# Kernel optimization log

Measured on AMD Instinct MI355X. Metric: run time of the kernel, lower is better.

Reference implementation:

```python
import jax, jax.numpy as jnp
import numpy as np

DIM = 768
HEADS = 12
HEAD_DIM = DIM // HEADS
SCALE = HEAD_DIM ** (-0.5)


def setup_inputs() -> dict:
    key = jax.random.key(0)
    k1, k2, k3, k4 = jax.random.split(key, 4)
    B, N = 2, 48 * 48
    x = jax.random.normal(k1, (B, N, DIM), dtype=jnp.float32)
    qkv_w = jax.random.normal(k2, (3 * DIM, DIM), dtype=jnp.float32) * (DIM ** -0.5)
    proj_w = jax.random.normal(k3, (DIM, DIM), dtype=jnp.float32) * (DIM ** -0.5)
    proj_b = jax.random.normal(k4, (DIM,), dtype=jnp.float32) * 0.02
    return {"x": x, "H": 48, "W": 48, "qkv_w": qkv_w, "proj_w": proj_w, "proj_b": proj_b}


def reference(x, H, W, qkv_w, proj_w, proj_b):
    B, N, C = x.shape
    h, d = HEADS, HEAD_DIM
    # qkv linear (no bias): [B,N,3C], then split into per-head q,k,v [B,h,N,d]
    qkv = jnp.einsum('bnc,fc->bnf', x, qkv_w)
    qkv = qkv.reshape(B, N, 3, h, d).transpose(2, 0, 3, 1, 4)
    q, k, v = qkv[0], qkv[1], qkv[2]
    attn = jnp.einsum('bhnd,bhmd->bhnm', q, k) * SCALE  # [B,h,N,N]
    attn = jax.nn.softmax(attn, axis=-1)
    out = jnp.einsum('bhnm,bhmd->bhnd', attn, v)  # [B,h,N,d]
    out = out.transpose(0, 2, 1, 3).reshape(B, N, C)
    out = jnp.einsum('bnc,fc->bnf', out, proj_w) + proj_b
    return out
```

## Files before the change

kernel.cpp:

```cpp
#include <hip/hip_runtime.h>

#define B_    2
#define N_    2304
#define C_    768
#define HEADS 12
#define D_    64
#define F3    2304
#define M_    (B_*N_)
#define SPLITS 2
#define KSPAN (N_/SPLITS)
#define QSCALE 0.18033688011112042f

typedef __attribute__((ext_vector_type(8)))  short bfrag;
typedef __attribute__((ext_vector_type(4)))  float ffrag;
typedef __attribute__((ext_vector_type(16))) float ffrag16;
typedef __attribute__((ext_vector_type(4)))  unsigned ufrag;

__device__ __forceinline__ short f2bf(float f) {
    unsigned u = __float_as_uint(f);
    u += 0x7fff + ((u >> 16) & 1);
    return (short)(u >> 16);
}

__device__ __forceinline__ void gl2lds16(const void* g, void* l) {
    __builtin_amdgcn_global_load_lds(
        (const __attribute__((address_space(1))) void*)g,
        (__attribute__((address_space(3))) void*)l, 16, 0, 0);
}

__device__ __forceinline__ unsigned pktrunc(float a, float b) {
    return __builtin_amdgcn_perm(__float_as_uint(a), __float_as_uint(b),
                                 0x03020706u);
}

__global__ __launch_bounds__(256) void cast_all(const float* __restrict__ x,
                                                const float* __restrict__ qw,
                                                const float* __restrict__ pw,
                                                short* __restrict__ dst) {
    const int nx4 = (M_*C_)/4, nq4 = (F3*C_)/4, np4 = (C_*C_)/4;
    int i = blockIdx.x * 256 + threadIdx.x;
    if (i >= nx4 + nq4 + np4) return;
    const float* src; int off;
    if (i < nx4)            { src = x;  off = i; }
    else if (i < nx4 + nq4) { src = qw; off = i - nx4; }
    else                    { src = pw; off = i - nx4 - nq4; }
    float4 v = ((const float4*)src)[off];
    short4 o;
    o.x = f2bf(v.x); o.y = f2bf(v.y); o.z = f2bf(v.z); o.w = f2bf(v.w);
    ((short4*)dst)[i] = o;
}

__global__ __launch_bounds__(256) void qkv_gemm(const short* __restrict__ xb,
                                                const short* __restrict__ wb,
                                                short* __restrict__ Qb,
                                                short* __restrict__ Kb,
                                                short* __restrict__ Vtb) {
    __shared__ short As[128*32];
    __shared__ short Bs[128*32];
    const int t = threadIdx.x;
    const int w = t >> 6, lane = t & 63;
    const int quad = lane >> 4, l15 = lane & 15;
    const int wr = w >> 1, wc = w & 1;
    const int m0 = blockIdx.y * 128, f0 = blockIdx.x * 128;

    ffrag acc[4][4] = {};

    for (int k0 = 0; k0 < C_; k0 += 32) {
        __syncthreads();
        #pragma unroll
        for (int r = 0; r < 2; ++r) {
            int seg = r*4 + w;
            int row = seg*16 + (lane >> 2);
            int kk  = (lane & 3) * 8;
            gl2lds16(xb + (size_t)(m0+row)*C_ + k0 + kk, As + seg*512);
            gl2lds16(wb + (size_t)(f0+row)*C_ + k0 + kk, Bs + seg*512);
        }
        __syncthreads();
        bfrag af[4], bf[4];
        #pragma unroll
        for (int i = 0; i < 4; ++i)
            af[i] = *(const bfrag*)(As + (wr*64 + i*16 + l15)*32 + quad*8);
        #pragma unroll
        for (int j = 0; j < 4; ++j)
            bf[j] = *(const bfrag*)(Bs + (wc*64 + j*16 + l15)*32 + quad*8);
        #pragma unroll
        for (int i = 0; i < 4; ++i)
            #pragma unroll
            for (int j = 0; j < 4; ++j)
                acc[i][j] = __builtin_amdgcn_mfma_f32_16x16x32_bf16(af[i], bf[j], acc[i][j], 0, 0, 0);
    }

    const int b   = m0 / N_;
    const int seg = f0 + wc*64;
    const int which = seg / C_;
    const int head  = (seg - which*C_) >> 6;
    const int bh    = b*HEADS + head;
    const int nbase = (m0 - b*N_) + wr*64 + quad*4;

    if (which == 0) {
        #pragma unroll
        for (int i = 0; i < 4; ++i) {
            int n0 = nbase + i*16;
            #pragma unroll
            for (int j = 0; j < 4; ++j) {
                int d = j*16 + l15;
                #pragma unroll
                for (int r = 0; r < 4; ++r)
                    Qb[((size_t)bh*N_ + n0 + r)*D_ + d] = f2bf(acc[i][j][r] * QSCALE);
            }
        }
    } else if (which == 1) {
        #pragma unroll
        for (int i = 0; i < 4; ++i) {
            int n0 = nbase + i*16;
            #pragma unroll
            for (int j = 0; j < 4; ++j) {
                int d = j*16 + l15;
                #pragma unroll
                for (int r = 0; r < 4; ++r)
                    Kb[((size_t)bh*N_ + n0 + r)*D_ + d] = f2bf(acc[i][j][r]);
            }
        }
    } else {
        #pragma unroll
        for (int i = 0; i < 4; ++i) {
            int n0 = nbase + i*16;
            #pragma unroll
            for (int j = 0; j < 4; ++j) {
                int d = j*16 + l15;
                short4 vv;
                vv.x = f2bf(acc[i][j][0]);
                vv.y = f2bf(acc[i][j][1]);
                vv.z = f2bf(acc[i][j][2]);
                vv.w = f2bf(acc[i][j][3]);
                *(short4*)(Vtb + ((size_t)bh*D_ + d)*N_ + n0) = vv;
            }
        }
    }
}

__global__ __launch_bounds__(128) void attn_mfma(const short* __restrict__ Qb,
                                                 const short* __restrict__ Kb,
                                                 const short* __restrict__ Vtb,
                                                 float* __restrict__ Opart,
                                                 float* __restrict__ lpart) {
    __shared__ short Qs[64*64];
    __shared__ short Ks[64*64];
    __shared__ short Vts[64*64];
    const int t = threadIdx.x;
    const int w = t >> 6, lane = t & 63;
    const int l31 = lane & 31, hi = lane >> 5;
    const int bh = blockIdx.x, q0 = blockIdx.y * 64;
    const int split = blockIdx.z;
    const int kbase = split * KSPAN;
    const size_t base = (size_t)bh * N_ * D_;
    const int lrow = lane >> 3;
    const int lc   = (lane & 7) ^ lrow;

    #pragma unroll
    for (int r = 0; r < 4; ++r) {
        int s = r*2 + w;
        int row = s*8 + lrow;
        gl2lds16(Qb + base + (size_t)(q0+row)*D_ + lc*8, Qs + s*512);
    }
    __syncthreads();

    bfrag qf[4];
    {
        int row = w*32 + l31, r7 = row & 7;
        #pragma unroll
        for (int kc = 0; kc < 4; ++kc)
            qf[kc] = *(const bfrag*)(Qs + row*64 + ((kc*2 + hi) ^ r7)*8);
    }

    bfrag vones;
    #pragma unroll
    for (int j = 0; j < 8; ++j) vones[j] = (short)0x3f80;

    ffrag16 oacc[2], lfr;
    #pragma unroll
    for (int r = 0; r < 16; ++r) { oacc[0][r] = 0.f; oacc[1][r] = 0.f; lfr[r] = 0.f; }

    for (int k0 = kbase; k0 < kbase + KSPAN; k0 += 64) {
        __syncthreads();
        #pragma unroll
        for (int r = 0; r < 4; ++r) {
            int s = r*2 + w;
            int row = s*8 + lrow;
            gl2lds16(Kb  + base + (size_t)(k0+row)*D_ + lc*8,    Ks  + s*512);
            gl2lds16(Vtb + (size_t)(bh*D_ + row)*N_ + k0 + lc*8, Vts + s*512);
        }
        __syncthreads();

        ufrag pfr[4];
        #pragma unroll
        for (int kt = 0; kt < 2; ++kt) {
            ffrag16 s;
            #pragma unroll
            for (int r = 0; r < 16; ++r) s[r] = 0.f;
            int row = kt*32 + l31, r7 = row & 7;
            #pragma unroll
            for (int kc = 0; kc < 4; ++kc) {
                bfrag kf = *(const bfrag*)(Ks + row*64 + ((kc*2 + hi) ^ r7)*8);
                s = __builtin_amdgcn_mfma_f32_32x32x16_bf16(kf, qf[kc], s, 0, 0, 0);
            }
            #pragma unroll
            for (int r = 0; r < 16; ++r)
                s[r] = __builtin_amdgcn_exp2f(s[r]);
            unsigned q01_0 = pktrunc(s[0],  s[1]),  q23_0 = pktrunc(s[2],  s[3]);
            unsigned q01_1 = pktrunc(s[4],  s[5]),  q23_1 = pktrunc(s[6],  s[7]);
            unsigned q01_2 = pktrunc(s[8],  s[9]),  q23_2 = pktrunc(s[10], s[11]);
            unsigned q01_3 = pktrunc(s[12], s[13]), q23_3 = pktrunc(s[14], s[15]);
            unsigned r0 = __shfl_xor(hi ? q01_0 : q01_1, 32, 64);
            unsigned r1 = __shfl_xor(hi ? q23_0 : q23_1, 32, 64);
            unsigned r2 = __shfl_xor(hi ? q01_2 : q01_3, 32, 64);
            unsigned r3 = __shfl_xor(hi ? q23_2 : q23_3, 32, 64);
            ufrag lo, hif;
            lo[0] = hi ? r0 : q01_0;  lo[1] = hi ? r1 : q23_0;
            lo[2] = hi ? q01_1 : r0;  lo[3] = hi ? q23_1 : r1;
            hif[0] = hi ? r2 : q01_2; hif[1] = hi ? r3 : q23_2;
            hif[2] = hi ? q01_3 : r2; hif[3] = hi ? q23_3 : r3;
            pfr[kt*2]     = lo;
            pfr[kt*2 + 1] = hif;
        }

        #pragma unroll
        for (int kc = 0; kc < 4; ++kc) {
            bfrag pf = __builtin_bit_cast(bfrag, pfr[kc]);
            #pragma unroll
            for (int dt = 0; dt < 2; ++dt) {
                int row = dt*32 + l31, r7 = row & 7;
                bfrag vf = *(const bfrag*)(Vts + row*64 + ((kc*2 + hi) ^ r7)*8);
                oacc[dt] = __builtin_amdgcn_mfma_f32_32x32x16_bf16(pf, vf, oacc[dt], 0, 0, 0);
            }
            lfr = __builtin_amdgcn_mfma_f32_32x32x16_bf16(pf, vones, lfr, 0, 0, 0);
        }
    }

    const int b = bh / HEADS, head = bh - b*HEADS;
    float* Op = Opart + (size_t)split * M_ * C_;
    float* lp = lpart + (size_t)split * (B_*HEADS) * N_;

    if (l31 == 0) {
        #pragma unroll
        for (int r = 0; r < 16; ++r) {
            int n = q0 + w*32 + (r & 3) + 8*(r >> 2) + 4*hi;
            lp[bh*N_ + n] = lfr[r];
        }
    }

    #pragma unroll
    for (int dt = 0; dt < 2; ++dt)
        #pragma unroll
        for (int r = 0; r < 16; ++r) {
            int n = q0 + w*32 + (r & 3) + 8*(r >> 2) + 4*hi;
            int c = head*D_ + dt*32 + l31;
            Op[((size_t)b*N_ + n)*C_ + c] = oacc[dt][r];
        }
}

__global__ __launch_bounds__(256) void attn_merge(const float* __restrict__ Opart,
                                                  const float* __restrict__ lpart,
                                                  short* __restrict__ Ob) {
    int i = blockIdx.x * 256 + threadIdx.x;
    int m = i / (C_/4);
    int c = (i - m*(C_/4)) * 4;
    int b = m / N_, n = m - b*N_;
    int bh = b*HEADS + (c >> 6);
    float4 o0 = ((const float4*)Opart)[i];
    float4 o1 = ((const float4*)(Opart + (size_t)M_*C_))[i];
    float l = lpart[bh*N_ + n] + lpart[(B_*HEADS)*N_ + bh*N_ + n];
    float inv = 1.f / l;
    short4 o;
    o.x = f2bf((o0.x + o1.x) * inv);
    o.y = f2bf((o0.y + o1.y) * inv);
    o.z = f2bf((o0.z + o1.z) * inv);
    o.w = f2bf((o0.w + o1.w) * inv);
    ((short4*)Ob)[i] = o;
}

__global__ __launch_bounds__(256) void proj_gemm(const short* __restrict__ Ab,
                                                 const short* __restrict__ wb,
                                                 const float* __restrict__ bias,
                                                 float* __restrict__ out) {
    __shared__ short As[128*32];
    __shared__ short Bs[128*32];
    const int t = threadIdx.x;
    const int w = t >> 6, lane = t & 63;
    const int quad = lane >> 4, l15 = lane & 15;
    const int wr = w >> 1, wc = w & 1;
    const int m0 = blockIdx.y * 128, f0 = blockIdx.x * 128;

    ffrag acc[4][4] = {};

    for (int k0 = 0; k0 < C_; k0 += 32) {
        __syncthreads();
        #pragma unroll
        for (int r = 0; r < 2; ++r) {
            int seg = r*4 + w;
            int row = seg*16 + (lane >> 2);
            int kk  = (lane & 3) * 8;
            gl2lds16(Ab + (size_t)(m0+row)*C_ + k0 + kk, As + seg*512);
            gl2lds16(wb + (size_t)(f0+row)*C_ + k0 + kk, Bs + seg*512);
        }
        __syncthreads();
        bfrag af[4], bf[4];
        #pragma unroll
        for (int i = 0; i < 4; ++i)
            af[i] = *(const bfrag*)(As + (wr*64 + i*16 + l15)*32 + quad*8);
        #pragma unroll
        for (int j = 0; j < 4; ++j)
            bf[j] = *(const bfrag*)(Bs + (wc*64 + j*16 + l15)*32 + quad*8);
        #pragma unroll
        for (int i = 0; i < 4; ++i)
            #pragma unroll
            for (int j = 0; j < 4; ++j)
                acc[i][j] = __builtin_amdgcn_mfma_f32_16x16x32_bf16(af[i], bf[j], acc[i][j], 0, 0, 0);
    }

    #pragma unroll
    for (int i = 0; i < 4; ++i) {
        int mbase = m0 + wr*64 + i*16 + quad*4;
        #pragma unroll
        for (int j = 0; j < 4; ++j) {
            int f = f0 + wc*64 + j*16 + l15;
            float bv = bias[f];
            #pragma unroll
            for (int r = 0; r < 4; ++r)
                out[(size_t)(mbase + r)*C_ + f] = acc[i][j][r] + bv;
        }
    }
}

extern "C" void kernel_launch(void* const* d_in, const int* in_sizes, int n_in,
                              void* d_out, int out_size, void* d_ws, size_t ws_size,
                              hipStream_t stream) {
    const float* x      = (const float*)d_in[0];
    const float* qkv_w  = (const float*)d_in[3];
    const float* proj_w = (const float*)d_in[4];
    const float* proj_b = (const float*)d_in[5];
    float* out = (float*)d_out;

    const size_t nx = (size_t)M_ * C_;
    const size_t nq = (size_t)F3 * C_;
    const size_t np = (size_t)C_ * C_;
    short* xb  = (short*)d_ws;
    short* qwb = xb  + nx;
    short* pwb = qwb + nq;
    short* Qb  = pwb + np;
    short* Kb  = Qb  + nx;
    short* Vtb = Kb  + nx;
    short* Ob  = Vtb + nx;
    float* Opart = (float*)(Ob + nx);
    float* lpart = Opart + (size_t)SPLITS * M_ * C_;

    const int ncast4 = (int)((nx + nq + np) / 4);
    cast_all<<<dim3((ncast4 + 255)/256), 256, 0, stream>>>(x, qkv_w, proj_w, xb);

    qkv_gemm<<<dim3(F3/128, M_/128), 256, 0, stream>>>(xb, qwb, Qb, Kb, Vtb);
    attn_mfma<<<dim3(B_*HEADS, N_/64, SPLITS), 128, 0, stream>>>(Qb, Kb, Vtb, Opart, lpart);
    attn_merge<<<dim3(((int)(nx/4) + 255)/256), 256, 0, stream>>>(Opart, lpart, Ob);
    proj_gemm<<<dim3(C_/128, M_/128), 256, 0, stream>>>(Ob, pwb, proj_b, out);
}
```

Measured before the change: 210.9 us.

## Widen K tiles in QKV GEMM and attention, add swizzled LDS layout

The QKV GEMM now stages a 64-wide K slice per iteration with an XOR-swizzled LDS layout, halving the number of barrier pairs and reducing bank conflicts. The attention kernel loads two 64-key K/V tiles per iteration into doubled LDS buffers, halving its sync count. It reuses the K buffer for the Q staging and adds a min-blocks-per-CU hint of 3. The cost is more LDS per block and possibly more register pressure under the occupancy hint.

```diff
diff --git a/kernel.cpp b/kernel.cpp
--- a/kernel.cpp
+++ b/kernel.cpp
@@ -55,39 +55,45 @@
                                                 short* __restrict__ Qb,
                                                 short* __restrict__ Kb,
                                                 short* __restrict__ Vtb) {
-    __shared__ short As[128*32];
-    __shared__ short Bs[128*32];
+    __shared__ short As[128*64];
+    __shared__ short Bs[128*64];
     const int t = threadIdx.x;
     const int w = t >> 6, lane = t & 63;
     const int quad = lane >> 4, l15 = lane & 15;
     const int wr = w >> 1, wc = w & 1;
     const int m0 = blockIdx.y * 128, f0 = blockIdx.x * 128;
+    const int lrow = lane >> 3;
+    const int lc   = (lane & 7) ^ lrow;
+    const int r7   = l15 & 7;
 
     ffrag acc[4][4] = {};
 
-    for (int k0 = 0; k0 < C_; k0 += 32) {
-        __syncthreads();
-        #pragma unroll
-        for (int r = 0; r < 2; ++r) {
+    for (int k0 = 0; k0 < C_; k0 += 64) {
+        __syncthreads();
+        #pragma unroll
+        for (int r = 0; r < 4; ++r) {
             int seg = r*4 + w;
-            int row = seg*16 + (lane >> 2);
-            int kk  = (lane & 3) * 8;
-            gl2lds16(xb + (size_t)(m0+row)*C_ + k0 + kk, As + seg*512);
-            gl2lds16(wb + (size_t)(f0+row)*C_ + k0 + kk, Bs + seg*512);
-        }
-        __syncthreads();
-        bfrag af[4], bf[4];
-        #pragma unroll
-        for (int i = 0; i < 4; ++i)
-            af[i] = *(const bfrag*)(As + (wr*64 + i*16 + l15)*32 + quad*8);
-        #pragma unroll
-        for (int j = 0; j < 4; ++j)
-            bf[j] = *(const bfrag*)(Bs + (wc*64 + j*16 + l15)*32 + quad*8);
-        #pragma unroll
-        for (int i = 0; i < 4; ++i)
+            int row = seg*8 + lrow;
+            gl2lds16(xb + (size_t)(m0+row)*C_ + k0 + lc*8, As + seg*512);
+            gl2lds16(wb + (size_t)(f0+row)*C_ + k0 + lc*8, Bs + seg*512);
+        }
+        __syncthreads();
+        #pragma unroll
+        for (int s = 0; s < 2; ++s) {
+            bfrag af[4], bf[4];
+            int slot = (s*4 + quad) ^ r7;
+            #pragma unroll
+            for (int i = 0; i < 4; ++i)
+                af[i] = *(const bfrag*)(As + (wr*64 + i*16 + l15)*64 + slot*8);
             #pragma unroll
             for (int j = 0; j < 4; ++j)
-                acc[i][j] = __builtin_amdgcn_mfma_f32_16x16x32_bf16(af[i], bf[j], acc[i][j], 0, 0, 0);
+                bf[j] = *(const bfrag*)(Bs + (wc*64 + j*16 + l15)*64 + slot*8);
+            #pragma unroll
+            for (int i = 0; i < 4; ++i)
+                #pragma unroll
+                for (int j = 0; j < 4; ++j)
+                    acc[i][j] = __builtin_amdgcn_mfma_f32_16x16x32_bf16(af[i], bf[j], acc[i][j], 0, 0, 0);
+        }
     }
 
     const int b   = m0 / N_;
@@ -139,14 +145,13 @@
     }
 }
 
-__global__ __launch_bounds__(128) void attn_mfma(const short* __restrict__ Qb,
-                                                 const short* __restrict__ Kb,
-                                                 const short* __restrict__ Vtb,
-                                                 float* __restrict__ Opart,
-                                                 float* __restrict__ lpart) {
-    __shared__ short Qs[64*64];
-    __shared__ short Ks[64*64];
-    __shared__ short Vts[64*64];
+__global__ __launch_bounds__(128, 3) void attn_mfma(const short* __restrict__ Qb,
+                                                    const short* __restrict__ Kb,
+                                                    const short* __restrict__ Vtb,
+                                                    float* __restrict__ Opart,
+                                                    float* __restrict__ lpart) {
+    __shared__ short Ks[2][64*64];
+    __shared__ short Vts[2][64*64];
     const int t = threadIdx.x;
     const int w = t >> 6, lane = t & 63;
     const int l31 = lane & 31, hi = lane >> 5;
@@ -161,7 +166,7 @@
     for (int r = 0; r < 4; ++r) {
         int s = r*2 + w;
         int row = s*8 + lrow;
-        gl2lds16(Qb + base + (size_t)(q0+row)*D_ + lc*8, Qs + s*512);
+        gl2lds16(Qb + base + (size_t)(q0+row)*D_ + lc*8, Ks[0] + s*512);
     }
     __syncthreads();
 
@@ -170,7 +175,7 @@
         int row = w*32 + l31, r7 = row & 7;
         #pragma unroll
         for (int kc = 0; kc < 4; ++kc)
-            qf[kc] = *(const bfrag*)(Qs + row*64 + ((kc*2 + hi) ^ r7)*8);
+            qf[kc] = *(const bfrag*)(Ks[0] + row*64 + ((kc*2 + hi) ^ r7)*8);
     }
 
     bfrag vones;
@@ -181,59 +186,64 @@
     #pragma unroll
     for (int r = 0; r < 16; ++r) { oacc[0][r] = 0.f; oacc[1][r] = 0.f; lfr[r] = 0.f; }
 
-    for (int k0 = kbase; k0 < kbase + KSPAN; k0 += 64) {
+    for (int k0 = kbase; k0 < kbase + KSPAN; k0 += 128) {
         __syncthreads();
         #pragma unroll
         for (int r = 0; r < 4; ++r) {
             int s = r*2 + w;
             int row = s*8 + lrow;
-            gl2lds16(Kb  + base + (size_t)(k0+row)*D_ + lc*8,    Ks  + s*512);
-            gl2lds16(Vtb + (size_t)(bh*D_ + row)*N_ + k0 + lc*8, Vts + s*512);
-        }
-        __syncthreads();
-
-        ufrag pfr[4];
-        #pragma unroll
-        for (int kt = 0; kt < 2; ++kt) {
-            ffrag16 s;
-            #pragma unroll
-            for (int r = 0; r < 16; ++r) s[r] = 0.f;
-            int row = kt*32 + l31, r7 = row & 7;
+            gl2lds16(Kb  + base + (size_t)(k0+row)*D_ + lc*8,         Ks[0]  + s*512);
+            gl2lds16(Vtb + (size_t)(bh*D_ + row)*N_ + k0 + lc*8,      Vts[0] + s*512);
+            gl2lds16(Kb  + base + (size_t)(k0+64+row)*D_ + lc*8,      Ks[1]  + s*512);
+            gl2lds16(Vtb + (size_t)(bh*D_ + row)*N_ + k0 + 64 + lc*8, Vts[1] + s*512);
+        }
+        __syncthreads();
+
+        #pragma unroll
+        for (int tb = 0; tb < 2; ++tb) {
+            ufrag pfr[4];
+            #pragma unroll
+            for (int kt = 0; kt < 2; ++kt) {
+                ffrag16 s;
+                #pragma unroll
+                for (int r = 0; r < 16; ++r) s[r] = 0.f;
+                int row = kt*32 + l31, r7 = row & 7;
+                #pragma unroll
+                for (int kc = 0; kc < 4; ++kc) {
+                    bfrag kf = *(const bfrag*)(Ks[tb] + row*64 + ((kc*2 + hi) ^ r7)*8);
+                    s = __builtin_amdgcn_mfma_f32_32x32x16_bf16(kf, qf[kc], s, 0, 0, 0);
+                }
+                #pragma unroll
+                for (int r = 0; r < 16; ++r)
+                    s[r] = __builtin_amdgcn_exp2f(s[r]);
+                unsigned q01_0 = pktrunc(s[0],  s[1]),  q23_0 = pktrunc(s[2],  s[3]);
+                unsigned q01_1 = pktrunc(s[4],  s[5]),  q23_1 = pktrunc(s[6],  s[7]);
+                unsigned q01_2 = pktrunc(s[8],  s[9]),  q23_2 = pktrunc(s[10], s[11]);
+                unsigned q01_3 = pktrunc(s[12], s[13]), q23_3 = pktrunc(s[14], s[15]);
+                unsigned r0 = __shfl_xor(hi ? q01_0 : q01_1, 32, 64);
+                unsigned r1 = __shfl_xor(hi ? q23_0 : q23_1, 32, 64);
+                unsigned r2 = __shfl_xor(hi ? q01_2 : q01_3, 32, 64);
+                unsigned r3 = __shfl_xor(hi ? q23_2 : q23_3, 32, 64);
+                ufrag lo, hif;
+                lo[0] = hi ? r0 : q01_0;  lo[1] = hi ? r1 : q23_0;
+                lo[2] = hi ? q01_1 : r0;  lo[3] = hi ? q23_1 : r1;
+                hif[0] = hi ? r2 : q01_2; hif[1] = hi ? r3 : q23_2;
+                hif[2] = hi ? q01_3 : r2; hif[3] = hi ? q23_3 : r3;
+                pfr[kt*2]     = lo;
+                pfr[kt*2 + 1] = hif;
+            }
+
             #pragma unroll
             for (int kc = 0; kc < 4; ++kc) {
-                bfrag kf = *(const bfrag*)(Ks + row*64 + ((kc*2 + hi) ^ r7)*8);
-                s = __builtin_amdgcn_mfma_f32_32x32x16_bf16(kf, qf[kc], s, 0, 0, 0);
-            }
-            #pragma unroll
-            for (int r = 0; r < 16; ++r)
-                s[r] = __builtin_amdgcn_exp2f(s[r]);
-            unsigned q01_0 = pktrunc(s[0],  s[1]),  q23_0 = pktrunc(s[2],  s[3]);
-            unsigned q01_1 = pktrunc(s[4],  s[5]),  q23_1 = pktrunc(s[6],  s[7]);
-            unsigned q01_2 = pktrunc(s[8],  s[9]),  q23_2 = pktrunc(s[10], s[11]);
-            unsigned q01_3 = pktrunc(s[12], s[13]), q23_3 = pktrunc(s[14], s[15]);
-            unsigned r0 = __shfl_xor(hi ? q01_0 : q01_1, 32, 64);
-            unsigned r1 = __shfl_xor(hi ? q23_0 : q23_1, 32, 64);
-            unsigned r2 = __shfl_xor(hi ? q01_2 : q01_3, 32, 64);
-            unsigned r3 = __shfl_xor(hi ? q23_2 : q23_3, 32, 64);
-            ufrag lo, hif;
-            lo[0] = hi ? r0 : q01_0;  lo[1] = hi ? r1 : q23_0;
-            lo[2] = hi ? q01_1 : r0;  lo[3] = hi ? q23_1 : r1;
-            hif[0] = hi ? r2 : q01_2; hif[1] = hi ? r3 : q23_2;
-            hif[2] = hi ? q01_3 : r2; hif[3] = hi ? q23_3 : r3;
-            pfr[kt*2]     = lo;
-            pfr[kt*2 + 1] = hif;
-        }
-
-        #pragma unroll
-        for (int kc = 0; kc < 4; ++kc) {
-            bfrag pf = __builtin_bit_cast(bfrag, pfr[kc]);
-            #pragma unroll
-            for (int dt = 0; dt < 2; ++dt) {
-                int row = dt*32 + l31, r7 = row & 7;
-                bfrag vf = *(const bfrag*)(Vts + row*64 + ((kc*2 + hi) ^ r7)*8);
-                oacc[dt] = __builtin_amdgcn_mfma_f32_32x32x16_bf16(pf, vf, oacc[dt], 0, 0, 0);
-            }
-            lfr = __builtin_amdgcn_mfma_f32_32x32x16_bf16(pf, vones, lfr, 0, 0, 0);
+                bfrag pf = __builtin_bit_cast(bfrag, pfr[kc]);
+                #pragma unroll
+                for (int dt = 0; dt < 2; ++dt) {
+                    int row = dt*32 + l31, r7 = row & 7;
+                    bfrag vf = *(const bfrag*)(Vts[tb] + row*64 + ((kc*2 + hi) ^ r7)*8);
+                    oacc[dt] = __builtin_amdgcn_mfma_f32_32x32x16_bf16(pf, vf, oacc[dt], 0, 0, 0);
+                }
+                lfr = __builtin_amdgcn_mfma_f32_32x32x16_bf16(pf, vones, lfr, 0, 0, 0);
+            }
         }
     }
 
```

Result: no change. 214.6 us (+1.7%).
